# Optimization experiments

Hardware: AMD Instinct MI355X
Metric: run time of the kernel (lower is better)

## Reference

```python
import jax, jax.numpy as jnp
import numpy as np


def setup_inputs() -> dict:
    key = jax.random.key(0)
    kY, kH = jax.random.split(key)
    B, M, L, S = 4, 512, 31, 2
    W = M + L - 1  # 542: dispersed measurement width
    Y = jax.random.uniform(kY, (B, M, W, S), dtype=jnp.float32)
    H = jax.random.uniform(kH, (B, M, M, L), dtype=jnp.float32)
    return {"Y": Y, "H": H}


def reference(Y, H):
    # Y: [B, M, W, S] measurement (W = M+L-1), H: [B, M, M, L] coded aperture
    B, M, W, S = Y.shape
    L = H.shape[-1]
    # tf.roll(Y, -i, axis=2)[:, :, 0:M] == Y[:, :, (j+i) % W] for j in [0, M)
    idx = (jnp.arange(M)[:, None] + jnp.arange(L)[None, :]) % W  # [M, L]
    Xs = Y[:, :, idx, :]                      # [B, M, M, L, S] shifted volume
    X = jnp.sum(H[..., None] * Xs, axis=4)    # sum over shots -> [B, M, M, L]
    return X / jnp.max(X)
```

## Files before the change

### kernel.cpp

```cpp
#include <hip/hip_runtime.h>
#include <hip/hip_bf16.h>

#define CB 4
#define CM 512
#define CL 31
#define CW 542
#define SLAB (CM * CL)
#define SLAB4 (SLAB / 4)
#define NBM (CB * CM)


__device__ __forceinline__ void stage_ysum(const float* __restrict__ Y, int bm, float* ysum) {
    const float2* y2 = (const float2*)(Y + (size_t)bm * CW * 2);
    for (int j = threadIdx.x; j < CW; j += 256) {
        float2 v = y2[j];
        ysum[j] = v.x + v.y;
    }
    __syncthreads();
}

__global__ __launch_bounds__(256) void cassi_max(
    const float* __restrict__ Y,
    const float* __restrict__ H,
    int* __restrict__ gmax)
{
    __shared__ float ysum[CW];
    int bm = blockIdx.x;
    stage_ysum(Y, bm, ysum);

    const float4* h4 = (const float4*)(H + (size_t)bm * SLAB);

    float mx = 0.0f;
    for (int i = threadIdx.x; i < SLAB4; i += 256) {
        float4 h = h4[i];
        unsigned f = (unsigned)i * 4u;
        unsigned n0 = f / 31u,        l0 = f - n0 * 31u;
        unsigned n1 = (f + 1) / 31u,  l1 = (f + 1) - n1 * 31u;
        unsigned n2 = (f + 2) / 31u,  l2 = (f + 2) - n2 * 31u;
        unsigned n3 = (f + 3) / 31u,  l3 = (f + 3) - n3 * 31u;
        float v0 = h.x * ysum[n0 + l0];
        float v1 = h.y * ysum[n1 + l1];
        float v2 = h.z * ysum[n2 + l2];
        float v3 = h.w * ysum[n3 + l3];
        mx = fmaxf(mx, fmaxf(fmaxf(v0, v1), fmaxf(v2, v3)));
    }

#pragma unroll
    for (int off = 32; off > 0; off >>= 1)
        mx = fmaxf(mx, __shfl_down(mx, off, 64));

    __shared__ float smax[4];
    int lane = threadIdx.x & 63;
    int wave = threadIdx.x >> 6;
    if (lane == 0) smax[wave] = mx;
    __syncthreads();
    if (threadIdx.x == 0) {
        float bmax = fmaxf(fmaxf(smax[0], smax[1]), fmaxf(smax[2], smax[3]));
        atomicMax(gmax, __float_as_int(bmax));
    }
}

__global__ __launch_bounds__(256) void cassi_out(
    const float* __restrict__ Y,
    const float* __restrict__ H,
    const int* __restrict__ gmax,
    float* __restrict__ out)
{
    __shared__ float ysum[CW];
    int bm = blockIdx.x;
    stage_ysum(Y, bm, ysum);

    float inv = 1.0f / __int_as_float(*gmax);

    const float4* h4 = (const float4*)(H + (size_t)bm * SLAB);
    float4* o4 = (float4*)(out + (size_t)bm * SLAB);

    for (int i = threadIdx.x; i < SLAB4; i += 256) {
        float4 h = h4[i];
        unsigned f = (unsigned)i * 4u;
        unsigned n0 = f / 31u,        l0 = f - n0 * 31u;
        unsigned n1 = (f + 1) / 31u,  l1 = (f + 1) - n1 * 31u;
        unsigned n2 = (f + 2) / 31u,  l2 = (f + 2) - n2 * 31u;
        unsigned n3 = (f + 3) / 31u,  l3 = (f + 3) - n3 * 31u;
        float4 o;
        o.x = h.x * ysum[n0 + l0] * inv;
        o.y = h.y * ysum[n1 + l1] * inv;
        o.z = h.z * ysum[n2 + l2] * inv;
        o.w = h.w * ysum[n3 + l3] * inv;
        o4[i] = o;
    }
}

extern "C" void kernel_launch(void* const* d_in, const int* in_sizes, int n_in,
                              void* d_out, int out_size, void* d_ws, size_t ws_size,
                              hipStream_t stream)
{
    const float* Y = (const float*)d_in[0];
    const float* H = (const float*)d_in[1];
    float* out = (float*)d_out;
    int* gmax = (int*)d_ws;

    hipMemsetAsync(d_ws, 0, sizeof(int), stream);

    cassi_max<<<NBM, 256, 0, stream>>>(Y, H, gmax);
    cassi_out<<<NBM, 256, 0, stream>>>(Y, H, gmax, out);
}
```

Before: 270.3 us.

## Replicate ysum in LDS, incremental index math, per-block max without atomics

Replaces the per-element divide-by-31 index math with incremental index state stepped each iteration, and replicates the ysum table four times in LDS so different thread groups read different copies, reducing bank conflicts. The global atomicMax and memset are dropped: each block writes its own max, and every block of the output kernel re-reduces all 2048 block maxima. Loops get a fixed trip count with partial unrolling and an occupancy hint in the launch bounds. This costs extra LDS per block and a redundant 2048-element reduction in every output block.

```diff
diff --git a/kernel.cpp b/kernel.cpp
--- a/kernel.cpp
+++ b/kernel.cpp
@@ -1,93 +1,158 @@
 #include <hip/hip_runtime.h>
-#include <hip/hip_bf16.h>
 
 #define CB 4
 #define CM 512
 #define CL 31
 #define CW 542
-#define SLAB (CM * CL)
+#define SLAB  (CM * CL)
 #define SLAB4 (SLAB / 4)
-#define NBM (CB * CM)
+#define NBM   (CB * CM)
+#define CPAD  543
 
 
-__device__ __forceinline__ void stage_ysum(const float* __restrict__ Y, int bm, float* ysum) {
-    const float2* y2 = (const float2*)(Y + (size_t)bm * CW * 2);
+__device__ __forceinline__ void stage_ysum(const float* __restrict__ Y, int bm,
+                                           float* __restrict__ ys) {
+    const float2* y2 = (const float2*)(Y + (size_t)bm * (CW * 2));
     for (int j = threadIdx.x; j < CW; j += 256) {
         float2 v = y2[j];
-        ysum[j] = v.x + v.y;
+        float s = v.x + v.y;
+        ys[j]            = s;
+        ys[j + CPAD]     = s;
+        ys[j + 2 * CPAD] = s;
+        ys[j + 3 * CPAD] = s;
     }
-    __syncthreads();
 }
 
-__global__ __launch_bounds__(256) void cassi_max(
+struct IdxState {
+    int l0;
+    int i0;
+};
+
+__device__ __forceinline__ IdxState idx_init(int tid) {
+    unsigned f = 4u * (unsigned)tid;
+    unsigned n = f / 31u;
+    IdxState s;
+    s.l0 = (int)(f - n * 31u);
+    s.i0 = (int)n + s.l0;
+    return s;
+}
+
+__device__ __forceinline__ void idx_quad(const IdxState& s,
+                                         int& i0, int& i1, int& i2, int& i3) {
+    i0 = s.i0;
+    i1 = s.i0 + ((s.l0 >= 30) ? 1 - 30 : 1);
+    i2 = s.i0 + ((s.l0 >= 29) ? 2 - 30 : 2);
+    i3 = s.i0 + ((s.l0 >= 28) ? 3 - 30 : 3);
+}
+
+__device__ __forceinline__ void idx_step(IdxState& s) {
+    bool w = (s.l0 == 30);
+    s.i0 += w ? 4 : 34;
+    s.l0  = w ? 0 : (s.l0 + 1);
+}
+
+__global__ __launch_bounds__(256, 8) void cassi_max(
     const float* __restrict__ Y,
     const float* __restrict__ H,
-    int* __restrict__ gmax)
+    float* __restrict__ blockmax)
 {
-    __shared__ float ysum[CW];
-    int bm = blockIdx.x;
+    __shared__ float ysum[4 * CPAD];
+    __shared__ float smax[4];
+    const int bm  = blockIdx.x;
+    const int tid = threadIdx.x;
+
     stage_ysum(Y, bm, ysum);
+    __syncthreads();
 
+    const float* ys = ysum + ((tid >> 3) & 3) * CPAD;
     const float4* h4 = (const float4*)(H + (size_t)bm * SLAB);
 
+    IdxState st = idx_init(tid);
     float mx = 0.0f;
-    for (int i = threadIdx.x; i < SLAB4; i += 256) {
-        float4 h = h4[i];
-        unsigned f = (unsigned)i * 4u;
-        unsigned n0 = f / 31u,        l0 = f - n0 * 31u;
-        unsigned n1 = (f + 1) / 31u,  l1 = (f + 1) - n1 * 31u;
-        unsigned n2 = (f + 2) / 31u,  l2 = (f + 2) - n2 * 31u;
-        unsigned n3 = (f + 3) / 31u,  l3 = (f + 3) - n3 * 31u;
-        float v0 = h.x * ysum[n0 + l0];
-        float v1 = h.y * ysum[n1 + l1];
-        float v2 = h.z * ysum[n2 + l2];
-        float v3 = h.w * ysum[n3 + l3];
+
+#pragma unroll 5
+    for (int k = 0; k < 15; ++k) {
+        float4 h = h4[tid + (k << 8)];
+        int i0, i1, i2, i3;
+        idx_quad(st, i0, i1, i2, i3);
+        float v0 = h.x * ys[i0];
+        float v1 = h.y * ys[i1];
+        float v2 = h.z * ys[i2];
+        float v3 = h.w * ys[i3];
+        mx = fmaxf(mx, fmaxf(fmaxf(v0, v1), fmaxf(v2, v3)));
+        idx_step(st);
+    }
+    if (tid < 128) {
+        float4 h = h4[tid + 15 * 256];
+        int i0, i1, i2, i3;
+        idx_quad(st, i0, i1, i2, i3);
+        float v0 = h.x * ys[i0];
+        float v1 = h.y * ys[i1];
+        float v2 = h.z * ys[i2];
+        float v3 = h.w * ys[i3];
         mx = fmaxf(mx, fmaxf(fmaxf(v0, v1), fmaxf(v2, v3)));
     }
 
 #pragma unroll
     for (int off = 32; off > 0; off >>= 1)
         mx = fmaxf(mx, __shfl_down(mx, off, 64));
-
-    __shared__ float smax[4];
-    int lane = threadIdx.x & 63;
-    int wave = threadIdx.x >> 6;
-    if (lane == 0) smax[wave] = mx;
+    if ((tid & 63) == 0) smax[tid >> 6] = mx;
     __syncthreads();
-    if (threadIdx.x == 0) {
-        float bmax = fmaxf(fmaxf(smax[0], smax[1]), fmaxf(smax[2], smax[3]));
-        atomicMax(gmax, __float_as_int(bmax));
-    }
+    if (tid == 0)
+        blockmax[bm] = fmaxf(fmaxf(smax[0], smax[1]), fmaxf(smax[2], smax[3]));
 }
 
-__global__ __launch_bounds__(256) void cassi_out(
+__global__ __launch_bounds__(256, 8) void cassi_out(
     const float* __restrict__ Y,
     const float* __restrict__ H,
-    const int* __restrict__ gmax,
+    const float* __restrict__ blockmax,
     float* __restrict__ out)
 {
-    __shared__ float ysum[CW];
-    int bm = blockIdx.x;
+    __shared__ float ysum[4 * CPAD];
+    __shared__ float sm[4];
+    const int bm  = blockIdx.x;
+    const int tid = threadIdx.x;
+
     stage_ysum(Y, bm, ysum);
 
-    float inv = 1.0f / __int_as_float(*gmax);
+    float m = 0.0f;
+    for (int j = tid; j < NBM; j += 256) m = fmaxf(m, blockmax[j]);
+#pragma unroll
+    for (int off = 32; off > 0; off >>= 1)
+        m = fmaxf(m, __shfl_down(m, off, 64));
+    if ((tid & 63) == 0) sm[tid >> 6] = m;
+    __syncthreads();
+    const float inv = 1.0f / fmaxf(fmaxf(sm[0], sm[1]), fmaxf(sm[2], sm[3]));
 
+    const float* ys = ysum + ((tid >> 3) & 3) * CPAD;
     const float4* h4 = (const float4*)(H + (size_t)bm * SLAB);
     float4* o4 = (float4*)(out + (size_t)bm * SLAB);
 
-    for (int i = threadIdx.x; i < SLAB4; i += 256) {
-        float4 h = h4[i];
-        unsigned f = (unsigned)i * 4u;
-        unsigned n0 = f / 31u,        l0 = f - n0 * 31u;
-        unsigned n1 = (f + 1) / 31u,  l1 = (f + 1) - n1 * 31u;
-        unsigned n2 = (f + 2) / 31u,  l2 = (f + 2) - n2 * 31u;
-        unsigned n3 = (f + 3) / 31u,  l3 = (f + 3) - n3 * 31u;
+    IdxState st = idx_init(tid);
+
+#pragma unroll 5
+    for (int k = 0; k < 15; ++k) {
+        float4 h = h4[tid + (k << 8)];
+        int i0, i1, i2, i3;
+        idx_quad(st, i0, i1, i2, i3);
         float4 o;
-        o.x = h.x * ysum[n0 + l0] * inv;
-        o.y = h.y * ysum[n1 + l1] * inv;
-        o.z = h.z * ysum[n2 + l2] * inv;
-        o.w = h.w * ysum[n3 + l3] * inv;
-        o4[i] = o;
+        o.x = h.x * ys[i0] * inv;
+        o.y = h.y * ys[i1] * inv;
+        o.z = h.z * ys[i2] * inv;
+        o.w = h.w * ys[i3] * inv;
+        o4[tid + (k << 8)] = o;
+        idx_step(st);
+    }
+    if (tid < 128) {
+        float4 h = h4[tid + 15 * 256];
+        int i0, i1, i2, i3;
+        idx_quad(st, i0, i1, i2, i3);
+        float4 o;
+        o.x = h.x * ys[i0] * inv;
+        o.y = h.y * ys[i1] * inv;
+        o.z = h.z * ys[i2] * inv;
+        o.w = h.w * ys[i3] * inv;
+        o4[tid + 15 * 256] = o;
     }
 }
 
@@ -98,10 +163,8 @@
     const float* Y = (const float*)d_in[0];
     const float* H = (const float*)d_in[1];
     float* out = (float*)d_out;
-    int* gmax = (int*)d_ws;
+    float* blockmax = (float*)d_ws;
 
-    hipMemsetAsync(d_ws, 0, sizeof(int), stream);
-
-    cassi_max<<<NBM, 256, 0, stream>>>(Y, H, gmax);
-    cassi_out<<<NBM, 256, 0, stream>>>(Y, H, gmax, out);
+    cassi_max<<<NBM, 256, 0, stream>>>(Y, H, blockmax);
+    cassi_out<<<NBM, 256, 0, stream>>>(Y, H, blockmax, out);
 }
```

Result: faster. 259.5 us (-4.0%).
